# Performance work log

Hardware: AMD Instinct MI355X
Metric: run time of the kernel (lower is better)

## Reference

```python
import jax, jax.numpy as jnp
import numpy as np

B, N, HID = 2, 2048, 1024
H, DH = 16, 64

def apply_rope(x, rope):
    # x: [B,H,N,D], rope: [B,N,D] interpreted as interleaved (cos, sin) pairs
    Bx, Hx, Nx, D = x.shape
    xp = x.reshape(Bx, Hx, Nx, D // 2, 2)
    rp = rope.reshape(Bx, 1, Nx, D // 2, 2)
    cos, sin = rp[..., 0], rp[..., 1]
    x0, x1 = xp[..., 0], xp[..., 1]
    out = jnp.stack([x0 * cos - x1 * sin, x1 * cos + x0 * sin], axis=-1)
    return out.reshape(Bx, Hx, Nx, D)


def setup_inputs() -> dict:
    key = jax.random.key(0)
    k1, k2, k3, k4 = jax.random.split(key, 4)
    x = jax.random.normal(k1, (B, N, HID), dtype=jnp.float32)
    rope = jax.random.normal(k2, (B, N, DH), dtype=jnp.float32)
    Wqkv = jax.random.normal(k3, (3 * H * DH, HID), dtype=jnp.float32) * (HID ** -0.5)
    Wout = jax.random.normal(k4, (HID, H * DH), dtype=jnp.float32) * ((H * DH) ** -0.5)
    return {"x": x, "rope": rope, "Wqkv": Wqkv, "Wout": Wout}


def reference(x, rope, Wqkv, Wout):
    scale = DH ** -0.5
    qkv = jnp.einsum('bnd,ed->bne', x, Wqkv)          # [B,N,3*H*DH]
    qkv = qkv.reshape(B, N, 3, H, DH)
    qkv = jnp.transpose(qkv, (2, 0, 3, 1, 4))          # [3,B,H,N,DH]
    q, k, v = qkv[0], qkv[1], qkv[2]
    q = apply_rope(q, rope)
    k = apply_rope(k, rope)
    attn = jnp.einsum('bhnd,bhmd->bhnm', q, k) * scale  # [B,H,N,N]
    attn = jax.nn.softmax(attn, axis=-1)
    out = jnp.einsum('bhnm,bhmd->bhnd', attn, v)        # [B,H,N,DH]
    out = jnp.transpose(out, (0, 2, 1, 3)).reshape(B, N, H * DH)
    return jnp.einsum('bne,de->bnd', out, Wout)
```

## Files before the change

kernel.cpp:

```cpp
#include <hip/hip_runtime.h>
#include <stdint.h>
#include <stddef.h>

typedef __bf16 bf16;
typedef __bf16 bf16x2 __attribute__((ext_vector_type(2)));
typedef __bf16 bf16x4 __attribute__((ext_vector_type(4)));
typedef __bf16 bf16x8 __attribute__((ext_vector_type(8)));
typedef float f32x2 __attribute__((ext_vector_type(2)));
typedef float f32x4 __attribute__((ext_vector_type(4)));
typedef float f32x16 __attribute__((ext_vector_type(16)));

constexpr int Bb = 2, Nn = 2048, HID = 1024, Hh = 16, DH = 64;
constexpr int MTOK = Bb * Nn;
constexpr int E3 = 3 * Hh * DH;

__global__ void cast3_kernel(const float* __restrict__ x, const float* __restrict__ wqkv,
                             const float* __restrict__ wout,
                             bf16* __restrict__ xb, bf16* __restrict__ wqkvb,
                             bf16* __restrict__ woutb) {
  constexpr int N1 = MTOK * HID / 4;
  constexpr int N2 = N1 + E3 * HID / 4;
  int i = blockIdx.x * 256 + threadIdx.x;
  const float* src;
  bf16* dst;
  int off;
  if (i < N1)      { src = x;    dst = xb;    off = i; }
  else if (i < N2) { src = wqkv; dst = wqkvb; off = i - N1; }
  else             { src = wout; dst = woutb; off = i - N2; }
  f32x4 v = reinterpret_cast<const f32x4*>(src)[off];
  bf16x4 o;
#pragma unroll
  for (int j = 0; j < 4; ++j) o[j] = (bf16)v[j];
  reinterpret_cast<bf16x4*>(dst)[off] = o;
}

template <bool OUT_BF16>
__global__ __launch_bounds__(256) void gemm_bt(const bf16* __restrict__ A,
                                               const bf16* __restrict__ Bt,
                                               void* __restrict__ Cp,
                                               int M, int N, int K) {
  __shared__ __align__(16) bf16 As[2][128 * 32];
  __shared__ __align__(16) bf16 Bs[2][128 * 32];
  const int tid = threadIdx.x;
  const int lane = tid & 63;
  const int wave = tid >> 6;
  const int wr = wave >> 1, wc = wave & 1;
  const int bm = blockIdx.x, bn = blockIdx.y;
  const int frow = lane & 15;
  const int fk = (lane >> 4) * 8;
  const int c0 = wave * 128 + lane;

  f32x4 acc[4][4] = {};

  for (int k0 = 0; k0 < K; k0 += 64) {
#pragma unroll
    for (int hk = 0; hk < 2; ++hk)
#pragma unroll
      for (int i = 0; i < 2; ++i) {
        int c = c0 + i * 64;
        int row = c >> 2;
        int col = (c & 3) * 8;
        const bf16* ga = A + (size_t)(bm * 128 + row) * K + k0 + hk * 32 + col;
        const bf16* gb = Bt + (size_t)(bn * 128 + row) * K + k0 + hk * 32 + col;
        __builtin_amdgcn_global_load_lds((const __attribute__((address_space(1))) void*)ga,
                                         (__attribute__((address_space(3))) void*)(As[hk] + c * 8),
                                         16, 0, 0);
        __builtin_amdgcn_global_load_lds((const __attribute__((address_space(1))) void*)gb,
                                         (__attribute__((address_space(3))) void*)(Bs[hk] + c * 8),
                                         16, 0, 0);
      }
    __syncthreads();
#pragma unroll
    for (int hk = 0; hk < 2; ++hk) {
      bf16x8 af[4], bfr[4];
#pragma unroll
      for (int m = 0; m < 4; ++m)
        af[m] = *reinterpret_cast<const bf16x8*>(As[hk] + (wr * 64 + m * 16 + frow) * 32 + fk);
#pragma unroll
      for (int n = 0; n < 4; ++n)
        bfr[n] = *reinterpret_cast<const bf16x8*>(Bs[hk] + (wc * 64 + n * 16 + frow) * 32 + fk);
#pragma unroll
      for (int m = 0; m < 4; ++m)
#pragma unroll
        for (int n = 0; n < 4; ++n)
          acc[m][n] = __builtin_amdgcn_mfma_f32_16x16x32_bf16(af[m], bfr[n], acc[m][n], 0, 0, 0);
    }
    __syncthreads();
  }

  const int r0 = bm * 128 + wr * 64;
  const int cc0 = bn * 128 + wc * 64;
#pragma unroll
  for (int m = 0; m < 4; ++m)
#pragma unroll
    for (int n = 0; n < 4; ++n)
#pragma unroll
      for (int r = 0; r < 4; ++r) {
        int row = r0 + m * 16 + (lane >> 4) * 4 + r;
        int col = cc0 + n * 16 + frow;
        if (OUT_BF16)
          ((bf16*)Cp)[(size_t)row * N + col] = (bf16)acc[m][n][r];
        else
          ((float*)Cp)[(size_t)row * N + col] = acc[m][n][r];
      }
}

__device__ __forceinline__ int kappa(int a) {
  return (((a >> 2) ^ (a >> 3)) & 1) ? (a ^ 12) : a;
}

__global__ __launch_bounds__(256) void rope_pack(const bf16* __restrict__ qkvb,
                                                 const float* __restrict__ rope,
                                                 bf16* __restrict__ qpk,
                                                 bf16* __restrict__ kpk,
                                                 bf16* __restrict__ vpk) {
  __shared__ bf16 qs[128][66];
  __shared__ bf16 ks[128][66];
  __shared__ bf16 vs[128][66];
  const int bh = blockIdx.y;
  const int b = bh >> 4;
  const int h = bh & 15;
  const int n0 = blockIdx.x * 128;
  const int t = threadIdx.x;

  constexpr float QS = 0.125f * 1.44269504088896340736f;

  for (int it = 0; it < 16; ++it) {
    int p = it * 256 + t;
    int nl = p >> 5, i = p & 31;
    int n = n0 + nl;
    size_t rowbase = (size_t)(b * Nn + n);
    const bf16* src = qkvb + rowbase * E3 + h * DH + 2 * i;
    f32x2 cs = *reinterpret_cast<const f32x2*>(rope + rowbase * DH + 2 * i);
    float c = cs[0], sn = cs[1];
    bf16x2 qv = *reinterpret_cast<const bf16x2*>(src);
    bf16x2 kv = *reinterpret_cast<const bf16x2*>(src + HID);
    bf16x2 vv = *reinterpret_cast<const bf16x2*>(src + 2 * HID);
    float q0 = (float)qv[0], q1 = (float)qv[1];
    float k0 = (float)kv[0], k1 = (float)kv[1];
    qs[nl][2 * i]     = (bf16)((q0 * c - q1 * sn) * QS);
    qs[nl][2 * i + 1] = (bf16)((q1 * c + q0 * sn) * QS);
    ks[nl][2 * i]     = (bf16)(k0 * c - k1 * sn);
    ks[nl][2 * i + 1] = (bf16)(k1 * c + k0 * sn);
    vs[nl][2 * i]     = vv[0];
    vs[nl][2 * i + 1] = vv[1];
  }
  __syncthreads();

  const int lane2 = t & 63;
  const int dd = t >> 6;
  const int lo2 = lane2 & 31, hi2 = lane2 >> 5;
  const int lok = kappa(lo2);
#pragma unroll
  for (int kbq = 0; kbq < 4; ++kbq) {
    int col = dd * 16 + hi2 * 8;
    bf16x8 q8 = *reinterpret_cast<const bf16x8*>(&qs[kbq * 32 + lo2][col]);
    bf16x8 k8 = *reinterpret_cast<const bf16x8*>(&ks[kbq * 32 + lok][col]);
    size_t base = ((((size_t)bh * 64 + (n0 >> 5) + kbq) * 4 + dd) * 64 + lane2) * 8;
    *reinterpret_cast<bf16x8*>(qpk + base) = q8;
    *reinterpret_cast<bf16x8*>(kpk + base) = k8;
  }

#pragma unroll
  for (int wi = 0; wi < 4; ++wi) {
    int id = wi * 256 + t;
    int lane3 = id & 63;
    int sub = id >> 6;
    int kt = sub >> 3, dt = (sub >> 2) & 1, kbi = sub & 3;
    int lo3 = lane3 & 31, hi3 = lane3 >> 5;
    bf16x8 v8;
#pragma unroll
    for (int j = 0; j < 8; ++j)
      v8[j] = vs[kt * 64 + kbi * 16 + hi3 * 8 + j][dt * 32 + lo3];
    size_t vbase = ((((size_t)bh * 32 + (n0 >> 6) + kt) * 8 + dt * 4 + kbi) * 64 + lane3) * 8;
    *reinterpret_cast<bf16x8*>(vpk + vbase) = v8;
  }
}

__global__ __launch_bounds__(256, 2) void attn_kernel(const bf16* __restrict__ qpk,
                                                      const bf16* __restrict__ kpk,
                                                      const bf16* __restrict__ vpk,
                                                      bf16* __restrict__ outb) {
  __shared__ __align__(16) char kvlds[2][32768];
  const int tid = threadIdx.x;
  const int lane = tid & 63;
  const int wave = tid >> 6;
  const int bid = blockIdx.x;
  const int xcd = bid & 7;
  const int idx = bid >> 3;
  const int bh = xcd * 4 + (idx >> 4);
  const int qt = idx & 15;
  const int b = bh >> 4, h = bh & 15;
  const int lo = lane & 31;
  const int hi = lane >> 5;
  const int q0 = qt * 128 + wave * 32;

  bf16x8 qf[4];
#pragma unroll
  for (int d = 0; d < 4; ++d)
    qf[d] = *reinterpret_cast<const bf16x8*>(
        qpk + ((((size_t)bh * 64 + qt * 4 + wave) * 4 + d) * 64 + lane) * 8);

  f32x16 o0 = {}, o1 = {};
  float lacc[16];
#pragma unroll
  for (int r = 0; r < 16; ++r) lacc[r] = 0.f;

  auto cvtpk = [](float a, float b) {
    unsigned w;
    asm("v_cvt_pk_bf16_f32 %0, %1, %2" : "=v"(w) : "v"(a), "v"(b));
    return w;
  };

  const bf16* kg = kpk + (size_t)bh * 131072 + wave * 512 + lane * 8;
  const bf16* vg = vpk + (size_t)bh * 131072 + wave * 512 + lane * 8;

  auto stage128 = [&](int til, int buf) {
    char* ld = &kvlds[buf][wave * 1024];
    const bf16* kk = kg + (size_t)til * 8192;
    const bf16* vv = vg + (size_t)til * 8192;
#pragma unroll
    for (int i = 0; i < 4; ++i) {
      __builtin_amdgcn_global_load_lds((const __attribute__((address_space(1))) void*)(kk + i * 2048),
                                       (__attribute__((address_space(3))) void*)(ld + i * 4096),
                                       16, 0, 0);
      __builtin_amdgcn_global_load_lds((const __attribute__((address_space(1))) void*)(vv + i * 2048),
                                       (__attribute__((address_space(3))) void*)(ld + 16384 + i * 4096),
                                       16, 0, 0);
    }
  };

  auto substep = [&](int cur, int s) {
    const char* base = &kvlds[cur][s * 8192 + lane * 16];
    bf16x8 kf[8], vf[8];
#pragma unroll
    for (int c = 0; c < 8; ++c) {
      kf[c] = *reinterpret_cast<const bf16x8*>(base + c * 1024);
      vf[c] = *reinterpret_cast<const bf16x8*>(base + 16384 + c * 1024);
    }

    f32x16 s0 = {}, s1 = {};
#pragma unroll
    for (int d = 0; d < 4; ++d) {
      s0 = __builtin_amdgcn_mfma_f32_32x32x16_bf16(kf[d], qf[d], s0, 0, 0, 0);
      s1 = __builtin_amdgcn_mfma_f32_32x32x16_bf16(kf[4 + d], qf[d], s1, 0, 0, 0);
    }

    float e[32];
#pragma unroll
    for (int r = 0; r < 16; ++r) e[r] = __builtin_amdgcn_exp2f(s0[r]);
#pragma unroll
    for (int r = 0; r < 16; ++r) e[16 + r] = __builtin_amdgcn_exp2f(s1[r]);

#pragma unroll
    for (int r = 0; r < 16; ++r) lacc[r] += e[r] + e[16 + r];

    union { unsigned w[4]; bf16x8 v8; } pb[4];
#pragma unroll
    for (int c = 0; c < 4; ++c)
#pragma unroll
      for (int w = 0; w < 4; ++w)
        pb[c].w[w] = cvtpk(e[c * 8 + 2 * w], e[c * 8 + 2 * w + 1]);

#pragma unroll
    for (int kbi = 0; kbi < 4; ++kbi) {
      o0 = __builtin_amdgcn_mfma_f32_32x32x16_bf16(vf[kbi], pb[kbi].v8, o0, 0, 0, 0);
      o1 = __builtin_amdgcn_mfma_f32_32x32x16_bf16(vf[4 + kbi], pb[kbi].v8, o1, 0, 0, 0);
    }
  };

  stage128(0, 0);
  __syncthreads();

  for (int t = 0; t < 16; ++t) {
    const int cur = t & 1;
    if (t < 15) stage128(t + 1, cur ^ 1);

    substep(cur, 0);
    substep(cur, 1);

    __syncthreads();
  }

  float lrun;
  {
    float u[8];
#pragma unroll
    for (int r = 0; r < 8; ++r) u[r] = lacc[r] + lacc[r + 8];
#pragma unroll
    for (int r = 0; r < 4; ++r) u[r] += u[r + 4];
    lrun = (u[0] + u[2]) + (u[1] + u[3]);
    lrun += __shfl_xor(lrun, 32);
  }
  float invl = 1.0f / lrun;
#pragma unroll
  for (int dt = 0; dt < 2; ++dt) {
#pragma unroll
    for (int g = 0; g < 4; ++g) {
      bf16x4 ov;
#pragma unroll
      for (int j = 0; j < 4; ++j) {
        float val = (dt ? o1[g * 4 + j] : o0[g * 4 + j]) * invl;
        ov[j] = (bf16)val;
      }
      int dh = dt * 32 + g * 8 + hi * 4;
      *reinterpret_cast<bf16x4*>(outb + (size_t)(b * Nn + q0 + lo) * HID + h * DH + dh) = ov;
    }
  }
}

extern "C" void kernel_launch(void* const* d_in, const int* in_sizes, int n_in,
                              void* d_out, int out_size, void* d_ws, size_t ws_size,
                              hipStream_t stream) {
  const float* x = (const float*)d_in[0];
  const float* rope = (const float*)d_in[1];
  const float* Wqkv = (const float*)d_in[2];
  const float* Wout = (const float*)d_in[3];
  float* out = (float*)d_out;

  char* w = (char*)d_ws;
  size_t off = 0;
  auto alloc = [&](size_t bytes) -> void* {
    void* p = w + off;
    off += (bytes + 255) & ~(size_t)255;
    return p;
  };
  bf16* xb    = (bf16*)alloc((size_t)MTOK * HID * 2);
  bf16* wqkvb = (bf16*)alloc((size_t)E3 * HID * 2);
  bf16* woutb = (bf16*)alloc((size_t)HID * HID * 2);
  bf16* qkvb  = (bf16*)alloc((size_t)MTOK * E3 * 2);
  bf16* qpk   = (bf16*)alloc((size_t)Bb * Hh * Nn * DH * 2);
  bf16* kpk   = (bf16*)alloc((size_t)Bb * Hh * Nn * DH * 2);
  bf16* vpk   = (bf16*)alloc((size_t)Bb * Hh * Nn * DH * 2);
  bf16* attno = (bf16*)alloc((size_t)MTOK * HID * 2);

  constexpr int CAST4 = (MTOK * HID + E3 * HID + HID * HID) / 4;
  cast3_kernel<<<CAST4 / 256, 256, 0, stream>>>(x, Wqkv, Wout, xb, wqkvb, woutb);

  gemm_bt<true><<<dim3(MTOK / 128, E3 / 128), 256, 0, stream>>>(xb, wqkvb, qkvb, MTOK, E3, HID);

  rope_pack<<<dim3(Nn / 128, Bb * Hh), 256, 0, stream>>>(qkvb, rope, qpk, kpk, vpk);

  attn_kernel<<<dim3(512), 256, 0, stream>>>(qpk, kpk, vpk, attno);

  gemm_bt<false><<<dim3(MTOK / 128, HID / 128), 256, 0, stream>>>(attno, woutb, out, MTOK, HID, HID);
}
```

Before: 117.8 us.

## Split attention KV sequence across two wave groups per block with LDS reduction

The attention block grows from 4 to 8 waves. Each pair of waves handles the same 32 queries, with each wave of the pair taking one half of the key/value sequence and staging 64-key tiles into its own double-buffered LDS region. At the end, the partial outputs and row sums from the second group go through LDS and are added by the first group before normalisation. The goal is more waves in flight to hide latency, at the cost of an extra reduction step, 32KB of LDS scratch traffic, and more register pressure from the launch bounds of 512 threads with 4 blocks.

```diff
diff --git a/kernel.cpp b/kernel.cpp
--- a/kernel.cpp
+++ b/kernel.cpp
@@ -177,14 +177,16 @@
   }
 }
 
-__global__ __launch_bounds__(256, 2) void attn_kernel(const bf16* __restrict__ qpk,
+__global__ __launch_bounds__(512, 4) void attn_kernel(const bf16* __restrict__ qpk,
                                                       const bf16* __restrict__ kpk,
                                                       const bf16* __restrict__ vpk,
                                                       bf16* __restrict__ outb) {
-  __shared__ __align__(16) char kvlds[2][32768];
+  __shared__ __align__(16) char kvlds[2][2][16384];
   const int tid = threadIdx.x;
   const int lane = tid & 63;
   const int wave = tid >> 6;
+  const int grp = wave >> 2;
+  const int wg = wave & 3;
   const int bid = blockIdx.x;
   const int xcd = bid & 7;
   const int idx = bid >> 3;
@@ -193,13 +195,13 @@
   const int b = bh >> 4, h = bh & 15;
   const int lo = lane & 31;
   const int hi = lane >> 5;
-  const int q0 = qt * 128 + wave * 32;
+  const int q0 = qt * 128 + wg * 32;
 
   bf16x8 qf[4];
 #pragma unroll
   for (int d = 0; d < 4; ++d)
     qf[d] = *reinterpret_cast<const bf16x8*>(
-        qpk + ((((size_t)bh * 64 + qt * 4 + wave) * 4 + d) * 64 + lane) * 8);
+        qpk + ((((size_t)bh * 64 + qt * 4 + wg) * 4 + d) * 64 + lane) * 8);
 
   f32x16 o0 = {}, o1 = {};
   float lacc[16];
@@ -212,31 +214,31 @@
     return w;
   };
 
-  const bf16* kg = kpk + (size_t)bh * 131072 + wave * 512 + lane * 8;
-  const bf16* vg = vpk + (size_t)bh * 131072 + wave * 512 + lane * 8;
-
-  auto stage128 = [&](int til, int buf) {
-    char* ld = &kvlds[buf][wave * 1024];
-    const bf16* kk = kg + (size_t)til * 8192;
-    const bf16* vv = vg + (size_t)til * 8192;
-#pragma unroll
-    for (int i = 0; i < 4; ++i) {
+  const bf16* kg = kpk + (size_t)bh * 131072 + wg * 512 + lane * 8;
+  const bf16* vg = vpk + (size_t)bh * 131072 + wg * 512 + lane * 8;
+
+  auto stage = [&](int til, int buf) {
+    char* ld = &kvlds[grp][buf][wg * 1024];
+    const bf16* kk = kg + (size_t)(grp * 16 + til) * 4096;
+    const bf16* vv = vg + (size_t)(grp * 16 + til) * 4096;
+#pragma unroll
+    for (int i = 0; i < 2; ++i) {
       __builtin_amdgcn_global_load_lds((const __attribute__((address_space(1))) void*)(kk + i * 2048),
                                        (__attribute__((address_space(3))) void*)(ld + i * 4096),
                                        16, 0, 0);
       __builtin_amdgcn_global_load_lds((const __attribute__((address_space(1))) void*)(vv + i * 2048),
-                                       (__attribute__((address_space(3))) void*)(ld + 16384 + i * 4096),
+                                       (__attribute__((address_space(3))) void*)(ld + 8192 + i * 4096),
                                        16, 0, 0);
     }
   };
 
-  auto substep = [&](int cur, int s) {
-    const char* base = &kvlds[cur][s * 8192 + lane * 16];
+  auto substep = [&](int cur) {
+    const char* base = &kvlds[grp][cur][lane * 16];
     bf16x8 kf[8], vf[8];
 #pragma unroll
     for (int c = 0; c < 8; ++c) {
       kf[c] = *reinterpret_cast<const bf16x8*>(base + c * 1024);
-      vf[c] = *reinterpret_cast<const bf16x8*>(base + 16384 + c * 1024);
+      vf[c] = *reinterpret_cast<const bf16x8*>(base + 8192 + c * 1024);
     }
 
     f32x16 s0 = {}, s1 = {};
@@ -269,16 +271,13 @@
     }
   };
 
-  stage128(0, 0);
+  stage(0, 0);
   __syncthreads();
 
   for (int t = 0; t < 16; ++t) {
     const int cur = t & 1;
-    if (t < 15) stage128(t + 1, cur ^ 1);
-
-    substep(cur, 0);
-    substep(cur, 1);
-
+    if (t < 15) stage(t + 1, cur ^ 1);
+    substep(cur);
     __syncthreads();
   }
 
@@ -292,19 +291,34 @@
     lrun = (u[0] + u[2]) + (u[1] + u[3]);
     lrun += __shfl_xor(lrun, 32);
   }
-  float invl = 1.0f / lrun;
-#pragma unroll
-  for (int dt = 0; dt < 2; ++dt) {
-#pragma unroll
-    for (int g = 0; g < 4; ++g) {
-      bf16x4 ov;
-#pragma unroll
-      for (int j = 0; j < 4; ++j) {
-        float val = (dt ? o1[g * 4 + j] : o0[g * 4 + j]) * invl;
-        ov[j] = (bf16)val;
+
+  float* scr = (float*)&kvlds[0][0][0];
+  if (grp == 1) {
+#pragma unroll
+    for (int r = 0; r < 16; ++r) scr[r * 256 + wg * 64 + lane] = o0[r];
+#pragma unroll
+    for (int r = 0; r < 16; ++r) scr[(16 + r) * 256 + wg * 64 + lane] = o1[r];
+    scr[8192 + wg * 64 + lane] = lrun;
+  }
+  __syncthreads();
+  if (grp == 0) {
+    float l1 = scr[8192 + wg * 64 + lane];
+    float invl = 1.0f / (lrun + l1);
+#pragma unroll
+    for (int dt = 0; dt < 2; ++dt) {
+#pragma unroll
+      for (int g = 0; g < 4; ++g) {
+        bf16x4 ov;
+#pragma unroll
+        for (int j = 0; j < 4; ++j) {
+          int r = g * 4 + j;
+          float mine = dt ? o1[r] : o0[r];
+          float partner = scr[(dt * 16 + r) * 256 + wg * 64 + lane];
+          ov[j] = (bf16)((mine + partner) * invl);
+        }
+        int dh = dt * 32 + g * 8 + hi * 4;
+        *reinterpret_cast<bf16x4*>(outb + (size_t)(b * Nn + q0 + lo) * HID + h * DH + dh) = ov;
       }
-      int dh = dt * 32 + g * 8 + hi * 4;
-      *reinterpret_cast<bf16x4*>(outb + (size_t)(b * Nn + q0 + lo) * HID + h * DH + dh) = ov;
     }
   }
 }
@@ -341,7 +355,7 @@
 
   rope_pack<<<dim3(Nn / 128, Bb * Hh), 256, 0, stream>>>(qkvb, rope, qpk, kpk, vpk);
 
-  attn_kernel<<<dim3(512), 256, 0, stream>>>(qpk, kpk, vpk, attno);
+  attn_kernel<<<dim3(512), 512, 0, stream>>>(qpk, kpk, vpk, attno);
 
   gemm_bt<false><<<dim3(MTOK / 128, HID / 128), 256, 0, stream>>>(attno, woutb, out, MTOK, HID, HID);
 }
```

New measurement: 117.8 us, median of 3. About the same (-0.0%).
